# Kernel tuning notes

Measured on AMD Instinct MI355X. Metric: run time of the kernel, lower is better.

Reference implementation:

```python
import jax, jax.numpy as jnp
import numpy as np

N = 4 * 1920 * 1080  # pixels per batch (4 full-HD frames)
NUM_CAMERAS = 8
NUM_FRAMES = 1000
RES_W, RES_H = 1920, 1080


def _sp_inv(x, min_val):
    # inverse softplus of (x - min_val), matching the torch init
    return float(np.log(np.expm1(max(1e-5, x - min_val))))


def setup_inputs() -> dict:
    key = jax.random.key(0)
    ks = jax.random.split(key, 8)
    rgb = jax.random.uniform(ks[0], (N, 3), dtype=jnp.float32)
    pixel_coords = jax.random.uniform(ks[1], (N, 2), dtype=jnp.float32) * jnp.array(
        [RES_W, RES_H], dtype=jnp.float32
    )
    camera_idcs = jax.random.randint(ks[2], (N,), 0, NUM_CAMERAS, dtype=jnp.int32)
    frame_idcs = jax.random.randint(ks[3], (N,), 0, NUM_FRAMES, dtype=jnp.int32)
    # small perturbations around the module's zero / identity-CRF init
    exposure_params = 0.1 * jax.random.normal(ks[4], (NUM_FRAMES,), dtype=jnp.float32)
    vignetting_params = 0.1 * jax.random.normal(
        ks[5], (NUM_CAMERAS, 3, 5), dtype=jnp.float32
    )
    color_params = 0.05 * jax.random.normal(ks[6], (NUM_FRAMES, 8), dtype=jnp.float32)
    crf_base = jnp.array(
        [_sp_inv(1.0, 0.3), _sp_inv(1.0, 0.3), _sp_inv(1.0, 0.1), 0.0],
        dtype=jnp.float32,
    )
    crf_params = crf_base[None, None, :] + 0.05 * jax.random.normal(
        ks[7], (NUM_CAMERAS, 3, 4), dtype=jnp.float32
    )
    return {
        "rgb": rgb,
        "pixel_coords": pixel_coords,
        "camera_idcs": camera_idcs,
        "frame_idcs": frame_idcs,
        "exposure_params": exposure_params,
        "vignetting_params": vignetting_params,
        "color_params": color_params,
        "crf_params": crf_params,
        "resolution_w": RES_W,
        "resolution_h": RES_H,
    }


def _ppisp(rgb, pixel_coords, camera_idcs, frame_idcs, exposure_params,
           vignetting_params, color_params, crf_params, w, h):
    # 1) per-frame exposure (log-exposure scalar)
    x = rgb * jnp.exp(exposure_params[frame_idcs])[:, None]  # [N,3]

    # 2) per-camera, per-channel radial vignetting: 2 center offsets + 3 alpha terms
    vp = vignetting_params[camera_idcs]  # [N,3,5]
    nx = pixel_coords[:, 0] / w - 0.5    # normalized coords in [-0.5, 0.5]
    ny = pixel_coords[:, 1] / h - 0.5
    dx = nx[:, None] - vp[..., 0]        # [N,3]
    dy = ny[:, None] - vp[..., 1]
    r2 = dx * dx + dy * dy
    vig = 1.0 + vp[..., 2] * r2 + vp[..., 3] * (r2 * r2) + vp[..., 4] * (r2 * r2 * r2)
    x = x * vig

    # 3) per-frame color transform: 2 WB gains (R,B) + 6 off-diagonal CCM terms
    cp = color_params[frame_idcs]  # [N,8]
    r = x[:, 0] * jnp.exp(cp[:, 0])
    g = x[:, 1]
    b = x[:, 2] * jnp.exp(cp[:, 1])
    o = cp[:, 2:8]
    x = jnp.stack(
        [
            r + o[:, 0] * g + o[:, 1] * b,
            o[:, 2] * r + g + o[:, 3] * b,
            o[:, 4] * r + o[:, 5] * g + b,
        ],
        axis=-1,
    )  # [N,3]

    # 4) per-camera, per-channel CRF (softplus-constrained; identity at init)
    kp = crf_params[camera_idcs]  # [N,3,4]
    k1 = 0.3 + jax.nn.softplus(kp[..., 0])
    k2 = 0.3 + jax.nn.softplus(kp[..., 1])
    k3 = 0.1 + jax.nn.softplus(kp[..., 2])
    k4 = kp[..., 3]
    xg = jnp.maximum(x, 1e-6) ** k3
    return k1 * xg / ((k1 - 1.0) * xg + k2) + k4


def reference(rgb, pixel_coords, camera_idcs, frame_idcs, exposure_params,
              vignetting_params, color_params, crf_params, resolution_w,
              resolution_h):
    w = jnp.float32(resolution_w)
    h = jnp.float32(resolution_h)
    return _ppisp(rgb, pixel_coords, camera_idcs, frame_idcs, exposure_params,
                  vignetting_params, color_params, crf_params, w, h)
```

## Files before the change

kernel.cpp:

```cpp
#include <hip/hip_runtime.h>

#define NUM_FRAMES 1000
#define NUM_CAM    8
#define CROW       12

#define WS_O5_OFF   16384
#define WS_CAM_OFF  18432
#define WS_REAL     19584
#define WS_PAD      32768

typedef _Float16 h8 __attribute__((ext_vector_type(8)));

struct __align__(4) F3 { float x, y, z; };

__device__ __forceinline__ float softplus_acc(float x) {
    return (x > 20.0f) ? x : log1pf(expf(x));
}

__device__ __forceinline__ float crf_pow(float m, float k3) {
    return __builtin_amdgcn_exp2f(k3 * __builtin_amdgcn_logf(fmaxf(m, 1e-6f)));
}

__global__ void build_tables(const float* __restrict__ expo,
                             const float* __restrict__ cp,
                             const float* __restrict__ vigp,
                             const float* __restrict__ crf,
                             unsigned char* __restrict__ ws)
{
    h8*       ftab = (h8*)ws;
    _Float16* o5t  = (_Float16*)(ws + WS_O5_OFF);
    float*    camt = (float*)(ws + WS_CAM_OFF);

    int t = blockIdx.x * blockDim.x + threadIdx.x;
    if (t < NUM_FRAMES) {
        float e = expo[t];
        const float* c = cp + t * 8;
        h8 row;
        row[0] = (_Float16)expf(e + c[0]);
        row[1] = (_Float16)expf(e);
        row[2] = (_Float16)expf(e + c[1]);
        row[3] = (_Float16)c[2];
        row[4] = (_Float16)c[3];
        row[5] = (_Float16)c[4];
        row[6] = (_Float16)c[5];
        row[7] = (_Float16)c[6];
        ftab[t] = row;
        o5t[t]  = (_Float16)c[7];
    }
    if (t < NUM_CAM * 3) {
        const float* v = vigp + t * 5;
        const float* k = crf + t * 4;
        float* d = camt + t * CROW;
        d[0] = v[0]; d[1] = v[1]; d[2] = v[2]; d[3] = v[3];
        d[4] = v[4];
        d[5] = 0.3f + softplus_acc(k[0]);
        d[6] = 0.3f + softplus_acc(k[1]);
        d[7] = 0.1f + softplus_acc(k[2]);
        d[8] = k[3];
        d[9] = 0.f; d[10] = 0.f; d[11] = 0.f;
    }
}

__device__ __forceinline__ void ppisp_px(
    float r, float g, float b, float px, float py,
    int cam, h8 fr, float o5, float invw, float invh,
    const float* __restrict__ s_cam,
    float* o)
{
    float er = (float)fr[0], eg = (float)fr[1], eb = (float)fr[2];
    float o0 = (float)fr[3], o1 = (float)fr[4], o2 = (float)fr[5];
    float o3 = (float)fr[6], o4 = (float)fr[7];

    float nx = px * invw - 0.5f;
    float ny = py * invh - 0.5f;

    float xin[3] = { r * er, g * eg, b * eb };
    float xv[3];
    float k1v[3], k2v[3], k3v[3], k4v[3];
#pragma unroll
    for (int ch = 0; ch < 3; ++ch) {
        const float* c = s_cam + (cam * 3 + ch) * CROW;
        float4 c0 = *(const float4*)(c);
        float4 c1 = *(const float4*)(c + 4);
        float  k4 = c[8];
        float dx = nx - c0.x;
        float dy = ny - c0.y;
        float r2 = __builtin_fmaf(dx, dx, dy * dy);
        float vg = __builtin_fmaf(__builtin_fmaf(__builtin_fmaf(c1.x, r2, c0.w), r2, c0.z), r2, 1.0f);
        xv[ch] = xin[ch] * vg;
        k1v[ch] = c1.y; k2v[ch] = c1.z; k3v[ch] = c1.w; k4v[ch] = k4;
    }

    float m[3];
    m[0] = __builtin_fmaf(o0, xv[1], __builtin_fmaf(o1, xv[2], xv[0]));
    m[1] = __builtin_fmaf(o2, xv[0], __builtin_fmaf(o3, xv[2], xv[1]));
    m[2] = __builtin_fmaf(o4, xv[0], __builtin_fmaf(o5, xv[1], xv[2]));

#pragma unroll
    for (int ch = 0; ch < 3; ++ch) {
        float xg  = crf_pow(m[ch], k3v[ch]);
        float den = __builtin_fmaf(k1v[ch] - 1.0f, xg, k2v[ch]);
        o[ch] = __builtin_fmaf(k1v[ch] * xg, __builtin_amdgcn_rcpf(den), k4v[ch]);
    }
}

__device__ __forceinline__ void ppisp_group(
    int gi, float4 r0, float4 r1, float4 r2, float4 p0, float4 p1,
    int4 cm, int4 fm, float invw, float invh,
    const h8* __restrict__ s_frame8, const _Float16* __restrict__ s_o5h,
    const float* __restrict__ s_cam, float4* __restrict__ out4)
{
    h8 f0 = s_frame8[fm.x];
    h8 f1 = s_frame8[fm.y];
    h8 f2 = s_frame8[fm.z];
    h8 f3 = s_frame8[fm.w];
    float o5a = (float)s_o5h[fm.x];
    float o5b = (float)s_o5h[fm.y];
    float o5c = (float)s_o5h[fm.z];
    float o5d = (float)s_o5h[fm.w];

    float a[3], bb[3], c[3], d[3];
    ppisp_px(r0.x, r0.y, r0.z, p0.x, p0.y, cm.x, f0, o5a, invw, invh, s_cam, a);
    ppisp_px(r0.w, r1.x, r1.y, p0.z, p0.w, cm.y, f1, o5b, invw, invh, s_cam, bb);
    ppisp_px(r1.z, r1.w, r2.x, p1.x, p1.y, cm.z, f2, o5c, invw, invh, s_cam, c);
    ppisp_px(r2.y, r2.z, r2.w, p1.z, p1.w, cm.w, f3, o5d, invw, invh, s_cam, d);

    out4[gi * 3 + 0] = make_float4(a[0], a[1], a[2], bb[0]);
    out4[gi * 3 + 1] = make_float4(bb[1], bb[2], c[0], c[1]);
    out4[gi * 3 + 2] = make_float4(c[2], d[0], d[1], d[2]);
}

__global__ __launch_bounds__(1024, 8)
void ppisp_px2(const float* __restrict__ rgb,
               const float* __restrict__ pc,
               const int*   __restrict__ cam_idx,
               const int*   __restrict__ frm_idx,
               const unsigned char* __restrict__ ws,
               const int*   __restrict__ resw_p,
               const int*   __restrict__ resh_p,
               float* __restrict__ out)
{
    __shared__ __align__(16) unsigned char s_tab[WS_PAD];

    int i0 = blockIdx.x * 2048 + threadIdx.x;
    int i1 = i0 + 1024;

    const int4* g = (const int4*)ws;
    int4 st0 = g[threadIdx.x];
    int4 st1 = g[threadIdx.x + 1024];

    int frm0 = frm_idx[i0];
    int frm1 = frm_idx[i1];
    int cam0 = cam_idx[i0];
    int cam1 = cam_idx[i1];
    const F3* rgb3 = (const F3*)rgb;
    const float2* pc2 = (const float2*)pc;
    F3 v0 = rgb3[i0];
    F3 v1 = rgb3[i1];
    float2 p0 = pc2[i0];
    float2 p1 = pc2[i1];
    int rw = *resw_p;
    int rh = *resh_p;

    int4* s = (int4*)s_tab;
    s[threadIdx.x] = st0;
    s[threadIdx.x + 1024] = st1;
    __syncthreads();

    const h8*       s_frame8 = (const h8*)s_tab;
    const _Float16* s_o5h    = (const _Float16*)(s_tab + WS_O5_OFF);
    const float*    s_cam    = (const float*)(s_tab + WS_CAM_OFF);

    float invw = 1.0f / (float)rw;
    float invh = 1.0f / (float)rh;

    F3* out3 = (F3*)out;

    {
        h8 fr = s_frame8[frm0];
        float o5 = (float)s_o5h[frm0];
        float o[3];
        ppisp_px(v0.x, v0.y, v0.z, p0.x, p0.y, cam0, fr, o5, invw, invh, s_cam, o);
        F3 w; w.x = o[0]; w.y = o[1]; w.z = o[2];
        out3[i0] = w;
    }
    {
        h8 fr = s_frame8[frm1];
        float o5 = (float)s_o5h[frm1];
        float o[3];
        ppisp_px(v1.x, v1.y, v1.z, p1.x, p1.y, cam1, fr, o5, invw, invh, s_cam, o);
        F3 w; w.x = o[0]; w.y = o[1]; w.z = o[2];
        out3[i1] = w;
    }
}

__global__ __launch_bounds__(256, 8)
void ppisp_main(const float* __restrict__ rgb,
                const float* __restrict__ pc,
                const int*   __restrict__ cam_idx,
                const int*   __restrict__ frm_idx,
                const unsigned char* __restrict__ ws,
                const int*   __restrict__ resw_p,
                const int*   __restrict__ resh_p,
                float* __restrict__ out,
                int n)
{
    __shared__ __align__(16) unsigned char s_tab[WS_REAL];
    {
        const int4* g = (const int4*)ws;
        int4* s = (int4*)s_tab;
#pragma unroll
        for (int i = threadIdx.x; i < WS_REAL / 16; i += 256) s[i] = g[i];
    }
    __syncthreads();

    const h8*       s_frame8 = (const h8*)s_tab;
    const _Float16* s_o5h    = (const _Float16*)(s_tab + WS_O5_OFF);
    const float*    s_cam    = (const float*)(s_tab + WS_CAM_OFF);

    float invw = 1.0f / (float)(*resw_p);
    float invh = 1.0f / (float)(*resh_p);

    const float4* rgb4 = (const float4*)rgb;
    const float4* pc4  = (const float4*)pc;
    const int4*   cam4 = (const int4*)cam_idx;
    const int4*   frm4 = (const int4*)frm_idx;
    float4* out4 = (float4*)out;

    int ngroups = n >> 2;
    int gi = blockIdx.x * 256 + threadIdx.x;

    if (gi < ngroups) {
        int4 fm = frm4[gi];
        int4 cm = cam4[gi];
        float4 r0 = rgb4[gi * 3 + 0];
        float4 r1 = rgb4[gi * 3 + 1];
        float4 r2 = rgb4[gi * 3 + 2];
        float4 p0 = pc4[gi * 2 + 0];
        float4 p1 = pc4[gi * 2 + 1];
        ppisp_group(gi, r0, r1, r2, p0, p1, cm, fm, invw, invh,
                    s_frame8, s_o5h, s_cam, out4);
    }

    int rem_start = ngroups << 2;
    int nrem = n - rem_start;
    if (blockIdx.x == 0 && (int)threadIdx.x < nrem) {
        int i = rem_start + threadIdx.x;
        int f = frm_idx[i];
        float o[3];
        ppisp_px(rgb[i * 3], rgb[i * 3 + 1], rgb[i * 3 + 2],
                 pc[i * 2], pc[i * 2 + 1],
                 cam_idx[i], s_frame8[f], (float)s_o5h[f], invw, invh, s_cam, o);
        out[i * 3 + 0] = o[0];
        out[i * 3 + 1] = o[1];
        out[i * 3 + 2] = o[2];
    }
}

__global__ __launch_bounds__(256, 8)
void ppisp_fallback(const float* __restrict__ rgb, const float* __restrict__ pc,
                    const int* __restrict__ cam_idx, const int* __restrict__ frm_idx,
                    const float* __restrict__ expo, const float* __restrict__ vigp,
                    const float* __restrict__ cp, const float* __restrict__ crf,
                    const int* __restrict__ resw_p, const int* __restrict__ resh_p,
                    float* __restrict__ out, int n)
{
    __shared__ __align__(16) h8 s_frame8[NUM_FRAMES];
    __shared__ _Float16 s_o5h[NUM_FRAMES];
    __shared__ __align__(16) float s_cam[NUM_CAM * 3 * CROW];

    for (int f = threadIdx.x; f < NUM_FRAMES; f += blockDim.x) {
        float e = expo[f];
        const float* c = cp + f * 8;
        h8 row;
        row[0] = (_Float16)expf(e + c[0]);
        row[1] = (_Float16)expf(e);
        row[2] = (_Float16)expf(e + c[1]);
        row[3] = (_Float16)c[2]; row[4] = (_Float16)c[3];
        row[5] = (_Float16)c[4]; row[6] = (_Float16)c[5];
        row[7] = (_Float16)c[6];
        s_frame8[f] = row;
        s_o5h[f] = (_Float16)c[7];
    }
    for (int rr = threadIdx.x; rr < NUM_CAM * 3; rr += blockDim.x) {
        const float* v = vigp + rr * 5;
        const float* k = crf + rr * 4;
        float* d = s_cam + rr * CROW;
        d[0] = v[0]; d[1] = v[1]; d[2] = v[2]; d[3] = v[3];
        d[4] = v[4];
        d[5] = 0.3f + softplus_acc(k[0]);
        d[6] = 0.3f + softplus_acc(k[1]);
        d[7] = 0.1f + softplus_acc(k[2]);
        d[8] = k[3];
        d[9] = 0.f; d[10] = 0.f; d[11] = 0.f;
    }
    __syncthreads();

    float invw = 1.0f / (float)(*resw_p);
    float invh = 1.0f / (float)(*resh_p);
    const float4* rgb4 = (const float4*)rgb;
    const float4* pc4  = (const float4*)pc;
    const int4* cam4 = (const int4*)cam_idx;
    const int4* frm4 = (const int4*)frm_idx;
    float4* out4 = (float4*)out;

    int ngroups = n >> 2;
    int stride = gridDim.x * blockDim.x;
    for (int gi = blockIdx.x * blockDim.x + threadIdx.x; gi < ngroups; gi += stride) {
        int4 fm = frm4[gi];
        int4 cm = cam4[gi];
        float4 r0 = rgb4[gi * 3 + 0], r1 = rgb4[gi * 3 + 1], r2 = rgb4[gi * 3 + 2];
        float4 p0 = pc4[gi * 2 + 0], p1 = pc4[gi * 2 + 1];
        ppisp_group(gi, r0, r1, r2, p0, p1, cm, fm, invw, invh,
                    s_frame8, s_o5h, s_cam, out4);
    }
    int rem_start = ngroups << 2;
    int nrem = n - rem_start;
    if (blockIdx.x == 0 && (int)threadIdx.x < nrem) {
        int i = rem_start + threadIdx.x;
        int f = frm_idx[i];
        float o[3];
        ppisp_px(rgb[i * 3], rgb[i * 3 + 1], rgb[i * 3 + 2], pc[i * 2], pc[i * 2 + 1],
                 cam_idx[i], s_frame8[f], (float)s_o5h[f], invw, invh, s_cam, o);
        out[i * 3 + 0] = o[0]; out[i * 3 + 1] = o[1]; out[i * 3 + 2] = o[2];
    }
}

extern "C" void kernel_launch(void* const* d_in, const int* in_sizes, int n_in,
                              void* d_out, int out_size, void* d_ws, size_t ws_size,
                              hipStream_t stream)
{
    const float* rgb  = (const float*)d_in[0];
    const float* pc   = (const float*)d_in[1];
    const int*   cam  = (const int*)d_in[2];
    const int*   frm  = (const int*)d_in[3];
    const float* expo = (const float*)d_in[4];
    const float* vigp = (const float*)d_in[5];
    const float* cp   = (const float*)d_in[6];
    const float* crf  = (const float*)d_in[7];
    const int*   resw = (const int*)d_in[8];
    const int*   resh = (const int*)d_in[9];
    float* out = (float*)d_out;

    int n = in_sizes[2];
    int ngroups = (n + 3) / 4;

    if (ws_size >= (size_t)WS_PAD && (n & 2047) == 0) {
        build_tables<<<dim3(4), dim3(256), 0, stream>>>(expo, cp, vigp, crf, (unsigned char*)d_ws);
        ppisp_px2<<<dim3(n / 2048), dim3(1024), 0, stream>>>(
            rgb, pc, cam, frm, (const unsigned char*)d_ws, resw, resh, out);
    } else if (ws_size >= (size_t)WS_REAL) {
        build_tables<<<dim3(4), dim3(256), 0, stream>>>(expo, cp, vigp, crf, (unsigned char*)d_ws);
        int blocks = (ngroups + 255) / 256;
        ppisp_main<<<dim3(blocks), dim3(256), 0, stream>>>(
            rgb, pc, cam, frm, (const unsigned char*)d_ws, resw, resh, out, n);
    } else {
        int blocks = (ngroups + 255) / 256;
        if (blocks > 2048) blocks = 2048;
        ppisp_fallback<<<dim3(blocks), dim3(256), 0, stream>>>(
            rgb, pc, cam, frm, expo, vigp, cp, crf, resw, resh, out, n);
    }
}
```

Measured before the change: 68.14 us.

## Fuse table construction into main kernel and process four pixels per thread

Result: faster. 64.44 us (-5.4%).

```diff
diff --git a/kernel.cpp b/kernel.cpp
--- a/kernel.cpp
+++ b/kernel.cpp
@@ -4,61 +4,23 @@
 #define NUM_CAM    8
 #define CROW       12
 
-#define WS_O5_OFF   16384
-#define WS_CAM_OFF  18432
-#define WS_REAL     19584
-#define WS_PAD      32768
-
 typedef _Float16 h8 __attribute__((ext_vector_type(8)));
 
 struct __align__(4) F3 { float x, y, z; };
 
-__device__ __forceinline__ float softplus_acc(float x) {
-    return (x > 20.0f) ? x : log1pf(expf(x));
-}
-
+#define LOG2E 1.44269504088896f
+#define LN2   0.69314718055995f
+
+__device__ __forceinline__ float softplus_fast(float x) {
+    if (x > 20.0f) return x;
+    float e = __builtin_amdgcn_exp2f(x * LOG2E);
+    return __builtin_amdgcn_logf(1.0f + e) * LN2;
+}
+__device__ __forceinline__ float exp_fast(float x) {
+    return __builtin_amdgcn_exp2f(x * LOG2E);
+}
 __device__ __forceinline__ float crf_pow(float m, float k3) {
     return __builtin_amdgcn_exp2f(k3 * __builtin_amdgcn_logf(fmaxf(m, 1e-6f)));
-}
-
-__global__ void build_tables(const float* __restrict__ expo,
-                             const float* __restrict__ cp,
-                             const float* __restrict__ vigp,
-                             const float* __restrict__ crf,
-                             unsigned char* __restrict__ ws)
-{
-    h8*       ftab = (h8*)ws;
-    _Float16* o5t  = (_Float16*)(ws + WS_O5_OFF);
-    float*    camt = (float*)(ws + WS_CAM_OFF);
-
-    int t = blockIdx.x * blockDim.x + threadIdx.x;
-    if (t < NUM_FRAMES) {
-        float e = expo[t];
-        const float* c = cp + t * 8;
-        h8 row;
-        row[0] = (_Float16)expf(e + c[0]);
-        row[1] = (_Float16)expf(e);
-        row[2] = (_Float16)expf(e + c[1]);
-        row[3] = (_Float16)c[2];
-        row[4] = (_Float16)c[3];
-        row[5] = (_Float16)c[4];
-        row[6] = (_Float16)c[5];
-        row[7] = (_Float16)c[6];
-        ftab[t] = row;
-        o5t[t]  = (_Float16)c[7];
-    }
-    if (t < NUM_CAM * 3) {
-        const float* v = vigp + t * 5;
-        const float* k = crf + t * 4;
-        float* d = camt + t * CROW;
-        d[0] = v[0]; d[1] = v[1]; d[2] = v[2]; d[3] = v[3];
-        d[4] = v[4];
-        d[5] = 0.3f + softplus_acc(k[0]);
-        d[6] = 0.3f + softplus_acc(k[1]);
-        d[7] = 0.1f + softplus_acc(k[2]);
-        d[8] = k[3];
-        d[9] = 0.f; d[10] = 0.f; d[11] = 0.f;
-    }
 }
 
 __device__ __forceinline__ void ppisp_px(
@@ -104,6 +66,119 @@
     }
 }
 
+__global__ __launch_bounds__(1024, 8)
+void ppisp_px4(const float* __restrict__ rgb,
+               const float* __restrict__ pc,
+               const int*   __restrict__ cam_idx,
+               const int*   __restrict__ frm_idx,
+               const float* __restrict__ expo,
+               const float* __restrict__ cp,
+               const float* __restrict__ vigp,
+               const float* __restrict__ crf,
+               const int*   __restrict__ resw_p,
+               const int*   __restrict__ resh_p,
+               float* __restrict__ out)
+{
+    __shared__ __align__(16) h8 s_frame8[NUM_FRAMES];
+    __shared__ _Float16 s_o5h[NUM_FRAMES];
+    __shared__ __align__(16) float s_cam[NUM_CAM * 3 * CROW];
+
+    int t = threadIdx.x;
+    int i0 = blockIdx.x * 4096 + t;
+    int i1 = i0 + 1024;
+    int i2 = i0 + 2048;
+    int i3 = i0 + 3072;
+
+    float e = 0.f;
+    float4 ca = make_float4(0.f, 0.f, 0.f, 0.f);
+    float4 cb = ca;
+    if (t < NUM_FRAMES) {
+        e  = expo[t];
+        ca = *(const float4*)(cp + t * 8);
+        cb = *(const float4*)(cp + t * 8 + 4);
+    }
+    float v0c = 0.f, v1c = 0.f, v2c = 0.f, v3c = 0.f, v4c = 0.f;
+    float k0c = 0.f, k1c = 0.f, k2c = 0.f, k3c = 0.f;
+    if (t < NUM_CAM * 3) {
+        const float* v = vigp + t * 5;
+        const float* k = crf + t * 4;
+        v0c = v[0]; v1c = v[1]; v2c = v[2]; v3c = v[3]; v4c = v[4];
+        k0c = k[0]; k1c = k[1]; k2c = k[2]; k3c = k[3];
+    }
+
+    int frm0 = frm_idx[i0], frm1 = frm_idx[i1], frm2 = frm_idx[i2], frm3 = frm_idx[i3];
+    int cam0 = cam_idx[i0], cam1 = cam_idx[i1], cam2 = cam_idx[i2], cam3 = cam_idx[i3];
+    const F3* rgb3 = (const F3*)rgb;
+    const float2* pc2 = (const float2*)pc;
+    F3 v0 = rgb3[i0], v1 = rgb3[i1], v2 = rgb3[i2], v3 = rgb3[i3];
+    float2 p0 = pc2[i0], p1 = pc2[i1], p2 = pc2[i2], p3 = pc2[i3];
+    int rw = *resw_p;
+    int rh = *resh_p;
+
+    if (t < NUM_FRAMES) {
+        h8 row;
+        row[0] = (_Float16)exp_fast(e + ca.x);
+        row[1] = (_Float16)exp_fast(e);
+        row[2] = (_Float16)exp_fast(e + ca.y);
+        row[3] = (_Float16)ca.z;
+        row[4] = (_Float16)ca.w;
+        row[5] = (_Float16)cb.x;
+        row[6] = (_Float16)cb.y;
+        row[7] = (_Float16)cb.z;
+        s_frame8[t] = row;
+        s_o5h[t] = (_Float16)cb.w;
+    }
+    if (t < NUM_CAM * 3) {
+        float* d = s_cam + t * CROW;
+        d[0] = v0c; d[1] = v1c; d[2] = v2c; d[3] = v3c;
+        d[4] = v4c;
+        d[5] = 0.3f + softplus_fast(k0c);
+        d[6] = 0.3f + softplus_fast(k1c);
+        d[7] = 0.1f + softplus_fast(k2c);
+        d[8] = k3c;
+        d[9] = 0.f; d[10] = 0.f; d[11] = 0.f;
+    }
+    __syncthreads();
+
+    float invw = 1.0f / (float)rw;
+    float invh = 1.0f / (float)rh;
+
+    F3* out3 = (F3*)out;
+
+    {
+        h8 fr = s_frame8[frm0];
+        float o5 = (float)s_o5h[frm0];
+        float o[3];
+        ppisp_px(v0.x, v0.y, v0.z, p0.x, p0.y, cam0, fr, o5, invw, invh, s_cam, o);
+        F3 w; w.x = o[0]; w.y = o[1]; w.z = o[2];
+        out3[i0] = w;
+    }
+    {
+        h8 fr = s_frame8[frm1];
+        float o5 = (float)s_o5h[frm1];
+        float o[3];
+        ppisp_px(v1.x, v1.y, v1.z, p1.x, p1.y, cam1, fr, o5, invw, invh, s_cam, o);
+        F3 w; w.x = o[0]; w.y = o[1]; w.z = o[2];
+        out3[i1] = w;
+    }
+    {
+        h8 fr = s_frame8[frm2];
+        float o5 = (float)s_o5h[frm2];
+        float o[3];
+        ppisp_px(v2.x, v2.y, v2.z, p2.x, p2.y, cam2, fr, o5, invw, invh, s_cam, o);
+        F3 w; w.x = o[0]; w.y = o[1]; w.z = o[2];
+        out3[i2] = w;
+    }
+    {
+        h8 fr = s_frame8[frm3];
+        float o5 = (float)s_o5h[frm3];
+        float o[3];
+        ppisp_px(v3.x, v3.y, v3.z, p3.x, p3.y, cam3, fr, o5, invw, invh, s_cam, o);
+        F3 w; w.x = o[0]; w.y = o[1]; w.z = o[2];
+        out3[i3] = w;
+    }
+}
+
 __device__ __forceinline__ void ppisp_group(
     int gi, float4 r0, float4 r1, float4 r2, float4 p0, float4 p1,
     int4 cm, int4 fm, float invw, float invh,
@@ -130,133 +205,6 @@
     out4[gi * 3 + 2] = make_float4(c[2], d[0], d[1], d[2]);
 }
 
-__global__ __launch_bounds__(1024, 8)
-void ppisp_px2(const float* __restrict__ rgb,
-               const float* __restrict__ pc,
-               const int*   __restrict__ cam_idx,
-               const int*   __restrict__ frm_idx,
-               const unsigned char* __restrict__ ws,
-               const int*   __restrict__ resw_p,
-               const int*   __restrict__ resh_p,
-               float* __restrict__ out)
-{
-    __shared__ __align__(16) unsigned char s_tab[WS_PAD];
-
-    int i0 = blockIdx.x * 2048 + threadIdx.x;
-    int i1 = i0 + 1024;
-
-    const int4* g = (const int4*)ws;
-    int4 st0 = g[threadIdx.x];
-    int4 st1 = g[threadIdx.x + 1024];
-
-    int frm0 = frm_idx[i0];
-    int frm1 = frm_idx[i1];
-    int cam0 = cam_idx[i0];
-    int cam1 = cam_idx[i1];
-    const F3* rgb3 = (const F3*)rgb;
-    const float2* pc2 = (const float2*)pc;
-    F3 v0 = rgb3[i0];
-    F3 v1 = rgb3[i1];
-    float2 p0 = pc2[i0];
-    float2 p1 = pc2[i1];
-    int rw = *resw_p;
-    int rh = *resh_p;
-
-    int4* s = (int4*)s_tab;
-    s[threadIdx.x] = st0;
-    s[threadIdx.x + 1024] = st1;
-    __syncthreads();
-
-    const h8*       s_frame8 = (const h8*)s_tab;
-    const _Float16* s_o5h    = (const _Float16*)(s_tab + WS_O5_OFF);
-    const float*    s_cam    = (const float*)(s_tab + WS_CAM_OFF);
-
-    float invw = 1.0f / (float)rw;
-    float invh = 1.0f / (float)rh;
-
-    F3* out3 = (F3*)out;
-
-    {
-        h8 fr = s_frame8[frm0];
-        float o5 = (float)s_o5h[frm0];
-        float o[3];
-        ppisp_px(v0.x, v0.y, v0.z, p0.x, p0.y, cam0, fr, o5, invw, invh, s_cam, o);
-        F3 w; w.x = o[0]; w.y = o[1]; w.z = o[2];
-        out3[i0] = w;
-    }
-    {
-        h8 fr = s_frame8[frm1];
-        float o5 = (float)s_o5h[frm1];
-        float o[3];
-        ppisp_px(v1.x, v1.y, v1.z, p1.x, p1.y, cam1, fr, o5, invw, invh, s_cam, o);
-        F3 w; w.x = o[0]; w.y = o[1]; w.z = o[2];
-        out3[i1] = w;
-    }
-}
-
-__global__ __launch_bounds__(256, 8)
-void ppisp_main(const float* __restrict__ rgb,
-                const float* __restrict__ pc,
-                const int*   __restrict__ cam_idx,
-                const int*   __restrict__ frm_idx,
-                const unsigned char* __restrict__ ws,
-                const int*   __restrict__ resw_p,
-                const int*   __restrict__ resh_p,
-                float* __restrict__ out,
-                int n)
-{
-    __shared__ __align__(16) unsigned char s_tab[WS_REAL];
-    {
-        const int4* g = (const int4*)ws;
-        int4* s = (int4*)s_tab;
-#pragma unroll
-        for (int i = threadIdx.x; i < WS_REAL / 16; i += 256) s[i] = g[i];
-    }
-    __syncthreads();
-
-    const h8*       s_frame8 = (const h8*)s_tab;
-    const _Float16* s_o5h    = (const _Float16*)(s_tab + WS_O5_OFF);
-    const float*    s_cam    = (const float*)(s_tab + WS_CAM_OFF);
-
-    float invw = 1.0f / (float)(*resw_p);
-    float invh = 1.0f / (float)(*resh_p);
-
-    const float4* rgb4 = (const float4*)rgb;
-    const float4* pc4  = (const float4*)pc;
-    const int4*   cam4 = (const int4*)cam_idx;
-    const int4*   frm4 = (const int4*)frm_idx;
-    float4* out4 = (float4*)out;
-
-    int ngroups = n >> 2;
-    int gi = blockIdx.x * 256 + threadIdx.x;
-
-    if (gi < ngroups) {
-        int4 fm = frm4[gi];
-        int4 cm = cam4[gi];
-        float4 r0 = rgb4[gi * 3 + 0];
-        float4 r1 = rgb4[gi * 3 + 1];
-        float4 r2 = rgb4[gi * 3 + 2];
-        float4 p0 = pc4[gi * 2 + 0];
-        float4 p1 = pc4[gi * 2 + 1];
-        ppisp_group(gi, r0, r1, r2, p0, p1, cm, fm, invw, invh,
-                    s_frame8, s_o5h, s_cam, out4);
-    }
-
-    int rem_start = ngroups << 2;
-    int nrem = n - rem_start;
-    if (blockIdx.x == 0 && (int)threadIdx.x < nrem) {
-        int i = rem_start + threadIdx.x;
-        int f = frm_idx[i];
-        float o[3];
-        ppisp_px(rgb[i * 3], rgb[i * 3 + 1], rgb[i * 3 + 2],
-                 pc[i * 2], pc[i * 2 + 1],
-                 cam_idx[i], s_frame8[f], (float)s_o5h[f], invw, invh, s_cam, o);
-        out[i * 3 + 0] = o[0];
-        out[i * 3 + 1] = o[1];
-        out[i * 3 + 2] = o[2];
-    }
-}
-
 __global__ __launch_bounds__(256, 8)
 void ppisp_fallback(const float* __restrict__ rgb, const float* __restrict__ pc,
                     const int* __restrict__ cam_idx, const int* __restrict__ frm_idx,
@@ -273,9 +221,9 @@
         float e = expo[f];
         const float* c = cp + f * 8;
         h8 row;
-        row[0] = (_Float16)expf(e + c[0]);
-        row[1] = (_Float16)expf(e);
-        row[2] = (_Float16)expf(e + c[1]);
+        row[0] = (_Float16)exp_fast(e + c[0]);
+        row[1] = (_Float16)exp_fast(e);
+        row[2] = (_Float16)exp_fast(e + c[1]);
         row[3] = (_Float16)c[2]; row[4] = (_Float16)c[3];
         row[5] = (_Float16)c[4]; row[6] = (_Float16)c[5];
         row[7] = (_Float16)c[6];
@@ -288,9 +236,9 @@
         float* d = s_cam + rr * CROW;
         d[0] = v[0]; d[1] = v[1]; d[2] = v[2]; d[3] = v[3];
         d[4] = v[4];
-        d[5] = 0.3f + softplus_acc(k[0]);
-        d[6] = 0.3f + softplus_acc(k[1]);
-        d[7] = 0.1f + softplus_acc(k[2]);
+        d[5] = 0.3f + softplus_fast(k[0]);
+        d[6] = 0.3f + softplus_fast(k[1]);
+        d[7] = 0.1f + softplus_fast(k[2]);
         d[8] = k[3];
         d[9] = 0.f; d[10] = 0.f; d[11] = 0.f;
     }
@@ -343,18 +291,12 @@
     float* out = (float*)d_out;
 
     int n = in_sizes[2];
-    int ngroups = (n + 3) / 4;
-
-    if (ws_size >= (size_t)WS_PAD && (n & 2047) == 0) {
-        build_tables<<<dim3(4), dim3(256), 0, stream>>>(expo, cp, vigp, crf, (unsigned char*)d_ws);
-        ppisp_px2<<<dim3(n / 2048), dim3(1024), 0, stream>>>(
-            rgb, pc, cam, frm, (const unsigned char*)d_ws, resw, resh, out);
-    } else if (ws_size >= (size_t)WS_REAL) {
-        build_tables<<<dim3(4), dim3(256), 0, stream>>>(expo, cp, vigp, crf, (unsigned char*)d_ws);
-        int blocks = (ngroups + 255) / 256;
-        ppisp_main<<<dim3(blocks), dim3(256), 0, stream>>>(
-            rgb, pc, cam, frm, (const unsigned char*)d_ws, resw, resh, out, n);
+
+    if ((n & 4095) == 0) {
+        ppisp_px4<<<dim3(n / 4096), dim3(1024), 0, stream>>>(
+            rgb, pc, cam, frm, expo, cp, vigp, crf, resw, resh, out);
     } else {
+        int ngroups = (n + 3) / 4;
         int blocks = (ngroups + 255) / 256;
         if (blocks > 2048) blocks = 2048;
         ppisp_fallback<<<dim3(blocks), dim3(256), 0, stream>>>(
```
